# Performance work log

Measured on AMD Instinct MI355X. Metric: run time of the kernel, lower is better.

The kernel has to match this reference:

```python
import jax, jax.numpy as jnp
import numpy as np

E, T, H, I = 8, 1024, 2048, 5632  # experts, tokens/expert, hidden, intermediate


def setup_inputs() -> dict:
    key = jax.random.key(0)
    k1, k2, k3 = jax.random.split(key, 3)
    permuted_hidden_states = jax.random.normal(k1, (E * T, H), dtype=jnp.float32)
    # per-expert weights; linear is x @ W with W[in, out] (same math as nn.Linear with W^T)
    w1 = jax.random.normal(k2, (E, H, 2 * I), dtype=jnp.float32) * 0.02
    w2 = jax.random.normal(k3, (E, I, H), dtype=jnp.float32) * 0.02
    tokens_per_expert = jnp.full((E,), T, dtype=jnp.int32)
    return {
        "permuted_hidden_states": permuted_hidden_states,
        "w1": w1,
        "w2": w2,
        "tokens_per_expert": tokens_per_expert,
    }


def reference(permuted_hidden_states, w1, w2, tokens_per_expert):
    # Tokens are contiguously segmented per expert; with equal counts (static T)
    # the per-expert loop becomes one batched (grouped) GEMM.
    x = permuted_hidden_states.reshape(E, T, H)
    fc1 = jnp.einsum('eth,ehf->etf', x, w1)          # [E, T, 2I]
    a, b = jnp.split(fc1, 2, axis=-1)                # GLU: chunk last dim
    inter = jax.nn.silu(a) * b                       # [E, T, I]
    out = jnp.einsum('eti,eih->eth', inter, w2)      # [E, T, H]
    return out.reshape(E * T, H)
```

## Files before the change

### kernel.cpp

```cpp
#include <hip/hip_runtime.h>
#include <hip/hip_bf16.h>


#define EXPERTS 8
#define TOK     1024
#define HID     2048
#define INTER   5632
#define I2      (2 * INTER)

typedef __bf16 bf16x8 __attribute__((ext_vector_type(8)));
typedef float  f32x4  __attribute__((ext_vector_type(4)));

#define G2(row) ((((row) >> 1) & 3) << 3)

__device__ __forceinline__ unsigned short f2bf(float f) {
    union { float f; unsigned u; } v; v.f = f;
    unsigned r = v.u + 0x7FFFu + ((v.u >> 16) & 1u);
    return (unsigned short)(r >> 16);
}

__device__ __forceinline__ void gload_lds16(const void* g, void* l) {
    __builtin_amdgcn_global_load_lds(
        (const __attribute__((address_space(1))) void*)g,
        (__attribute__((address_space(3))) void*)l, 16, 0, 0);
}

__device__ __forceinline__ bf16x8 ldfrag(const unsigned short* S, int R, int kb) {
    int off = R * 32 + (kb ^ G2(R));
    return *reinterpret_cast<const bf16x8*>(S + off);
}


__global__ __launch_bounds__(256) void k_cvt_x(const float* __restrict__ X,
                                               unsigned short* __restrict__ Xb) {
    size_t base = ((size_t)blockIdx.x * 256 + threadIdx.x) * 8;
    int row = (int)(base >> 11);
    int k   = (int)(base & (HID - 1));
    int kp  = k ^ G2(row);
    float4 v0 = *reinterpret_cast<const float4*>(X + base);
    float4 v1 = *reinterpret_cast<const float4*>(X + base + 4);
    uint4 o;
    o.x = (unsigned)f2bf(v0.x) | ((unsigned)f2bf(v0.y) << 16);
    o.y = (unsigned)f2bf(v0.z) | ((unsigned)f2bf(v0.w) << 16);
    o.z = (unsigned)f2bf(v1.x) | ((unsigned)f2bf(v1.y) << 16);
    o.w = (unsigned)f2bf(v1.z) | ((unsigned)f2bf(v1.w) << 16);
    *reinterpret_cast<uint4*>(Xb + (size_t)row * HID + kp) = o;
}

__global__ __launch_bounds__(256) void k_cvt_w1(const float* __restrict__ W1,
                                                unsigned short* __restrict__ W1T) {
    __shared__ unsigned short lds[64][72];
    const int bid = blockIdx.x;
    const int hb = bid % (HID / 64);
    const int pb = (bid / (HID / 64)) % (I2 / 64);
    const int e  = bid / ((HID / 64) * (I2 / 64));
    const int h0 = hb * 64, p0 = pb * 64, n0 = p0 >> 1;
    const float* w1e = W1 + (size_t)e * HID * I2;
    const int t = threadIdx.x;
#pragma unroll
    for (int it = 0; it < 16; ++it) {
        int lin   = it * 256 + t;
        int n_off = lin & 31;
        int c     = (lin >> 5) & 1;
        int h_off = lin >> 6;
        float v = w1e[(size_t)(h0 + h_off) * I2 + c * INTER + n0 + n_off];
        lds[2 * n_off + c][h_off] = f2bf(v);
    }
    __syncthreads();
    unsigned short* o = W1T + (size_t)e * I2 * HID;
#pragma unroll
    for (int it = 0; it < 4; ++it) {
        int lin = it * 256 + t;
        int r   = lin >> 4;
        int co  = (lin & 15) * 4;
        int cop = co ^ G2(r);
        ushort4 v = *reinterpret_cast<ushort4*>(&lds[r][co]);
        *reinterpret_cast<ushort4*>(o + (size_t)(p0 + r) * HID + h0 + cop) = v;
    }
}

__global__ __launch_bounds__(256) void k_cvt_w2(const float* __restrict__ W2,
                                                unsigned short* __restrict__ W2T) {
    __shared__ unsigned short lds[64][72];
    const int bid = blockIdx.x;
    const int ib = bid % (INTER / 64);
    const int hb = (bid / (INTER / 64)) % (HID / 64);
    const int e  = bid / ((INTER / 64) * (HID / 64));
    const int i0 = ib * 64, h0 = hb * 64;
    const float* w2e = W2 + (size_t)e * INTER * HID;
    const int t = threadIdx.x;
#pragma unroll
    for (int it = 0; it < 16; ++it) {
        int lin   = it * 256 + t;
        int h_off = lin & 63;
        int i_off = lin >> 6;
        float v = w2e[(size_t)(i0 + i_off) * HID + h0 + h_off];
        lds[h_off][i_off] = f2bf(v);
    }
    __syncthreads();
    unsigned short* o = W2T + (size_t)e * HID * INTER;
#pragma unroll
    for (int it = 0; it < 4; ++it) {
        int lin = it * 256 + t;
        int r   = lin >> 4;
        int co  = (lin & 15) * 4;
        int cop = co ^ G2(r);
        ushort4 v = *reinterpret_cast<ushort4*>(&lds[r][co]);
        *reinterpret_cast<ushort4*>(o + (size_t)(h0 + r) * INTER + i0 + cop) = v;
    }
}


__device__ __forceinline__ void stage24(const unsigned short* Ab, const unsigned short* Bb,
                                        int ktot, int k0, unsigned short* buf, int t) {
#pragma unroll
    for (int j = 0; j < 2; ++j) {
        int lin = j * 512 + t;
        int row = lin >> 2;
        int col = (lin & 3) * 8;
        gload_lds16(Ab + (size_t)row * ktot + k0 + col, buf + lin * 8);
    }
    {
        int row = t >> 2;
        int col = (t & 3) * 8;
        gload_lds16(Bb + (size_t)row * ktot + k0 + col, buf + 8192 + t * 8);
    }
}

#define MFMA_BF16(a, b, c) __builtin_amdgcn_mfma_f32_16x16x32_bf16(a, b, c, 0, 0, 0)

__device__ __forceinline__ void gemm_ring3(const unsigned short* Ab, const unsigned short* Bb,
                                           int ktot, int nkt, f32x4 (&acc)[4][4],
                                           unsigned short* lds, int t, int lane,
                                           int wr, int wc) {
    const int cl  = lane & 15;
    const int kb0 = (lane >> 4) << 3;

    stage24(Ab, Bb, ktot, 0,  lds,         t);
    stage24(Ab, Bb, ktot, 32, lds + 12288, t);

    int c_cur = 0, c_n2 = 2;
    for (int kt = 0; kt < nkt; ++kt) {
        if (kt + 1 < nkt) { asm volatile("s_waitcnt vmcnt(3)" ::: "memory"); }
        else              { asm volatile("s_waitcnt vmcnt(0)" ::: "memory"); }
        __builtin_amdgcn_s_barrier();
        asm volatile("" ::: "memory");

        unsigned short* Ac = lds + c_cur * 12288;
        unsigned short* Bc = Ac + 8192;

        if (kt + 2 < nkt)
            stage24(Ab, Bb, ktot, (kt + 2) * 32, lds + c_n2 * 12288, t);

        bf16x8 b[4], a[2];
#pragma unroll
        for (int n = 0; n < 4; ++n)
            b[n] = ldfrag(Bc, wc + n * 16 + cl, kb0);
        a[0] = ldfrag(Ac, wr + cl, kb0);

#pragma unroll
        for (int m = 0; m < 4; ++m) {
            if (m < 3)
                a[(m + 1) & 1] = ldfrag(Ac, wr + (m + 1) * 16 + cl, kb0);
            __builtin_amdgcn_s_setprio(1);
#pragma unroll
            for (int n = 0; n < 4; ++n)
                acc[m][n] = MFMA_BF16(a[m & 1], b[n], acc[m][n]);
            __builtin_amdgcn_s_setprio(0);
        }

        c_cur = (c_cur == 2) ? 0 : c_cur + 1;
        c_n2  = (c_n2  == 2) ? 0 : c_n2  + 1;
    }
}

__global__ __launch_bounds__(512, 4) void k_fc1_r3(const unsigned short* __restrict__ Xb,
                                                   const unsigned short* __restrict__ W1T,
                                                   unsigned short* __restrict__ inter) {
    extern __shared__ unsigned short lds[];
    const int bid = blockIdx.x;
    const int e   = bid & 7;
    const int idx = bid >> 3;
    const int mt  = idx & 3;
    const int nt  = idx >> 2;
    const int t = threadIdx.x, lane = t & 63, w = t >> 6;
    const int wr = (w >> 1) * 64;
    const int wc = (w & 1) * 64;
    const int m0 = e * TOK + mt * 256;
    const int n0 = nt * 128;
    const unsigned short* Ab = Xb  + (size_t)m0 * HID;
    const unsigned short* Bb = W1T + (size_t)e * I2 * HID + (size_t)n0 * HID;

    f32x4 acc[4][4];
#pragma unroll
    for (int i = 0; i < 4; ++i)
#pragma unroll
        for (int j = 0; j < 4; ++j) acc[i][j] = f32x4{0.f, 0.f, 0.f, 0.f};

    gemm_ring3(Ab, Bb, HID, HID / 32, acc, lds, t, lane, wr, wc);

    const int cl = lane & 15;
    const int r0 = (lane >> 4) << 2;
#pragma unroll
    for (int mf = 0; mf < 4; ++mf)
#pragma unroll
        for (int nf = 0; nf < 4; ++nf)
#pragma unroll
            for (int r = 0; r < 4; ++r) {
                float v  = acc[mf][nf][r];
                float pv = __shfl_xor(v, 1);
                if ((lane & 1) == 0) {
                    float s = v / (1.f + __expf(-v)) * pv;
                    int row = m0 + wr + mf * 16 + r0 + r;
                    int pc  = n0 + wc + nf * 16 + cl;
                    int c   = pc >> 1;
                    int c2  = (c & ~31) | ((c & 31) ^ G2(row));
                    inter[(size_t)row * INTER + c2] = f2bf(s);
                }
            }
}

__global__ __launch_bounds__(512, 4) void k_fc2_r3(const unsigned short* __restrict__ A,
                                                   const unsigned short* __restrict__ W2T,
                                                   float* __restrict__ out) {
    extern __shared__ unsigned short lds[];
    const int bid = blockIdx.x;
    const int e   = bid & 7;
    const int idx = bid >> 3;
    const int mt  = idx & 3;
    const int nt  = idx >> 2;
    const int t = threadIdx.x, lane = t & 63, w = t >> 6;
    const int wr = (w >> 1) * 64;
    const int wc = (w & 1) * 64;
    const int m0 = e * TOK + mt * 256;
    const int n0 = nt * 128;
    const unsigned short* Ab = A   + (size_t)m0 * INTER;
    const unsigned short* Bb = W2T + (size_t)e * HID * INTER + (size_t)n0 * INTER;

    f32x4 acc[4][4];
#pragma unroll
    for (int i = 0; i < 4; ++i)
#pragma unroll
        for (int j = 0; j < 4; ++j) acc[i][j] = f32x4{0.f, 0.f, 0.f, 0.f};

    gemm_ring3(Ab, Bb, INTER, INTER / 32, acc, lds, t, lane, wr, wc);

    const int cl = lane & 15;
    const int r0 = (lane >> 4) << 2;
#pragma unroll
    for (int mf = 0; mf < 4; ++mf)
#pragma unroll
        for (int nf = 0; nf < 4; ++nf)
#pragma unroll
            for (int r = 0; r < 4; ++r) {
                int row = m0 + wr + mf * 16 + r0 + r;
                int col = n0 + wc + nf * 16 + cl;
                out[(size_t)row * HID + col] = acc[mf][nf][r];
            }
}


#define BM  128
#define BK  64
#define LDK 72

__global__ __launch_bounds__(256) void k_fc1_glu_fb(
    const float* __restrict__ X, const float* __restrict__ W1,
    unsigned short* __restrict__ inter)
{
    __shared__ unsigned short As[BM][LDK];
    __shared__ unsigned short Bs[128][LDK];
    const int bid = blockIdx.x;
    const int nt  = bid % (INTER / 64);
    const int mt  = (bid / (INTER / 64)) % (TOK / BM);
    const int e   = bid / ((INTER / 64) * (TOK / BM));
    const int t = threadIdx.x, lane = t & 63, w = t >> 6;
    const int m0 = mt * BM;
    const int rowbase = e * TOK + m0;
    f32x4 acc[2][8];
#pragma unroll
    for (int i = 0; i < 2; ++i)
#pragma unroll
        for (int jj = 0; jj < 8; ++jj) acc[i][jj] = f32x4{0.f, 0.f, 0.f, 0.f};
    const int jcol = t & 127;
    const int hf   = t >> 7;
    const int gcol = (jcol < 64) ? (nt * 64 + jcol) : (INTER + nt * 64 + (jcol - 64));
    const float* w1e = W1 + (size_t)e * HID * I2;
    for (int k0 = 0; k0 < HID; k0 += BK) {
#pragma unroll
        for (int it = 0; it < 8; ++it) {
            int lin = it * 256 + t;
            int r   = lin >> 4;
            int kq  = (lin & 15) << 2;
            const float4 v = *reinterpret_cast<const float4*>(
                X + (size_t)(rowbase + r) * HID + k0 + kq);
            ushort4 o;
            o.x = f2bf(v.x); o.y = f2bf(v.y); o.z = f2bf(v.z); o.w = f2bf(v.w);
            *reinterpret_cast<ushort4*>(&As[r][kq]) = o;
        }
#pragma unroll
        for (int it = 0; it < 8; ++it) {
            int kq = hf * 4 + it * 8;
            const float* p = w1e + (size_t)(k0 + kq) * I2 + gcol;
            float v0 = p[0], v1 = p[I2], v2 = p[2 * I2], v3 = p[3 * I2];
            ushort4 o;
            o.x = f2bf(v0); o.y = f2bf(v1); o.z = f2bf(v2); o.w = f2bf(v3);
            *reinterpret_cast<ushort4*>(&Bs[jcol][kq]) = o;
        }
        __syncthreads();
#pragma unroll
        for (int kk = 0; kk < 2; ++kk) {
            const int kb = kk * 32 + ((lane >> 4) << 3);
            bf16x8 a0 = *reinterpret_cast<const bf16x8*>(&As[w * 32 + (lane & 15)][kb]);
            bf16x8 a1 = *reinterpret_cast<const bf16x8*>(&As[w * 32 + 16 + (lane & 15)][kb]);
#pragma unroll
            for (int nf = 0; nf < 8; ++nf) {
                bf16x8 b = *reinterpret_cast<const bf16x8*>(&Bs[nf * 16 + (lane & 15)][kb]);
                acc[0][nf] = MFMA_BF16(a0, b, acc[0][nf]);
                acc[1][nf] = MFMA_BF16(a1, b, acc[1][nf]);
            }
        }
        __syncthreads();
    }
    const int rl0 = w * 32 + ((lane >> 4) << 2);
    const int cl  = lane & 15;
#pragma unroll
    for (int mf = 0; mf < 2; ++mf)
#pragma unroll
        for (int nfa = 0; nfa < 4; ++nfa) {
            f32x4 va = acc[mf][nfa];
            f32x4 vb = acc[mf][nfa + 4];
#pragma unroll
            for (int r = 0; r < 4; ++r) {
                float a = va[r], b = vb[r];
                float s = a / (1.f + __expf(-a)) * b;
                int row = rowbase + rl0 + mf * 16 + r;
                int col = nt * 64 + nfa * 16 + cl;
                inter[(size_t)row * INTER + col] = f2bf(s);
            }
        }
}

__global__ __launch_bounds__(256) void k_fc2_fb(
    const unsigned short* __restrict__ inter, const float* __restrict__ W2,
    float* __restrict__ out)
{
    __shared__ unsigned short As[BM][LDK];
    __shared__ unsigned short Bs[128][LDK];
    const int bid = blockIdx.x;
    const int nt  = bid % (HID / 128);
    const int mt  = (bid / (HID / 128)) % (TOK / BM);
    const int e   = bid / ((HID / 128) * (TOK / BM));
    const int t = threadIdx.x, lane = t & 63, w = t >> 6;
    const int m0 = mt * BM;
    const int rowbase = e * TOK + m0;
    f32x4 acc[2][8];
#pragma unroll
    for (int i = 0; i < 2; ++i)
#pragma unroll
        for (int jj = 0; jj < 8; ++jj) acc[i][jj] = f32x4{0.f, 0.f, 0.f, 0.f};
    const int jcol = t & 127;
    const int hf   = t >> 7;
    const int gcol = nt * 128 + jcol;
    const float* w2e = W2 + (size_t)e * INTER * HID;
    for (int k0 = 0; k0 < INTER; k0 += BK) {
#pragma unroll
        for (int it = 0; it < 4; ++it) {
            int lin = it * 256 + t;
            int r   = lin >> 3;
            int kq  = (lin & 7) << 3;
            uint4 v = *reinterpret_cast<const uint4*>(
                inter + (size_t)(rowbase + r) * INTER + k0 + kq);
            *reinterpret_cast<uint4*>(&As[r][kq]) = v;
        }
#pragma unroll
        for (int it = 0; it < 8; ++it) {
            int kq = hf * 4 + it * 8;
            const float* p = w2e + (size_t)(k0 + kq) * HID + gcol;
            float v0 = p[0], v1 = p[HID], v2 = p[2 * HID], v3 = p[3 * HID];
            ushort4 o;
            o.x = f2bf(v0); o.y = f2bf(v1); o.z = f2bf(v2); o.w = f2bf(v3);
            *reinterpret_cast<ushort4*>(&Bs[jcol][kq]) = o;
        }
        __syncthreads();
#pragma unroll
        for (int kk = 0; kk < 2; ++kk) {
            const int kb = kk * 32 + ((lane >> 4) << 3);
            bf16x8 a0 = *reinterpret_cast<const bf16x8*>(&As[w * 32 + (lane & 15)][kb]);
            bf16x8 a1 = *reinterpret_cast<const bf16x8*>(&As[w * 32 + 16 + (lane & 15)][kb]);
#pragma unroll
            for (int nf = 0; nf < 8; ++nf) {
                bf16x8 b = *reinterpret_cast<const bf16x8*>(&Bs[nf * 16 + (lane & 15)][kb]);
                acc[0][nf] = MFMA_BF16(a0, b, acc[0][nf]);
                acc[1][nf] = MFMA_BF16(a1, b, acc[1][nf]);
            }
        }
        __syncthreads();
    }
    const int rl0 = w * 32 + ((lane >> 4) << 2);
    const int cl  = lane & 15;
#pragma unroll
    for (int mf = 0; mf < 2; ++mf)
#pragma unroll
        for (int nf = 0; nf < 8; ++nf) {
            f32x4 v = acc[mf][nf];
#pragma unroll
            for (int r = 0; r < 4; ++r) {
                int row = rowbase + rl0 + mf * 16 + r;
                int col = nt * 128 + nf * 16 + cl;
                out[(size_t)row * HID + col] = v[r];
            }
        }
}


extern "C" void kernel_launch(void* const* d_in, const int* in_sizes, int n_in,
                              void* d_out, int out_size, void* d_ws, size_t ws_size,
                              hipStream_t stream) {
    const float* X  = (const float*)d_in[0];
    const float* W1 = (const float*)d_in[1];
    const float* W2 = (const float*)d_in[2];
    float* out = (float*)d_out;

    const size_t XB_B  = (size_t)EXPERTS * TOK * HID * 2;
    const size_t W1T_B = (size_t)EXPERTS * I2 * HID * 2;
    const size_t W2T_B = (size_t)EXPERTS * HID * INTER * 2;
    const size_t INT_B = (size_t)EXPERTS * TOK * INTER * 2;
    const size_t need  = XB_B + W1T_B + W2T_B + INT_B;

    if (ws_size >= need) {
        unsigned short* Xb    = (unsigned short*)d_ws;
        unsigned short* w1t   = (unsigned short*)((char*)d_ws + XB_B);
        unsigned short* w2t   = (unsigned short*)((char*)d_ws + XB_B + W1T_B);
        unsigned short* inter = (unsigned short*)((char*)d_ws + XB_B + W1T_B + W2T_B);

        hipFuncSetAttribute((const void*)k_fc1_r3,
            hipFuncAttributeMaxDynamicSharedMemorySize, 73728);
        hipFuncSetAttribute((const void*)k_fc2_r3,
            hipFuncAttributeMaxDynamicSharedMemorySize, 73728);

        dim3 b256(256), b512(512);
        k_cvt_x <<<(EXPERTS * TOK * HID) / (256 * 8), b256, 0, stream>>>(X, Xb);
        k_cvt_w1<<<EXPERTS * (I2 / 64) * (HID / 64),   b256, 0, stream>>>(W1, w1t);
        k_cvt_w2<<<EXPERTS * (HID / 64) * (INTER / 64), b256, 0, stream>>>(W2, w2t);
        k_fc1_r3<<<EXPERTS * 4 * (I2 / 128),  b512, 73728, stream>>>(Xb, w1t, inter);
        k_fc2_r3<<<EXPERTS * 4 * (HID / 128), b512, 73728, stream>>>(inter, w2t, out);
    } else {
        unsigned short* inter = (unsigned short*)d_ws;
        dim3 b256(256);
        k_fc1_glu_fb<<<EXPERTS * (TOK / BM) * (INTER / 64), b256, 0, stream>>>(X, W1, inter);
        k_fc2_fb    <<<EXPERTS * (TOK / BM) * (HID / 128),  b256, 0, stream>>>(inter, W2, out);
    }
}
```

Baseline: 938.6 us.

## Fuse fp32-to-bf16 weight conversion into GEMM B-tile staging, drop transpose kernels

Removes the separate weight transpose/convert kernels and their bf16 workspace copies. Each GEMM now loads the fp32 weight columns straight from global memory into registers, converts them to bf16 and writes them swizzled into LDS, interleaving the GLU columns for fc1. This saves a full read and write pass over the weights. In exchange the GEMM reads twice the bytes per B tile (fp32), and each M-tile block re-converts the same weights. The strided per-thread loads are coalesced across threads along the column.

```diff
diff --git a/kernel.cpp b/kernel.cpp
--- a/kernel.cpp
+++ b/kernel.cpp
@@ -47,135 +47,105 @@
     *reinterpret_cast<uint4*>(Xb + (size_t)row * HID + kp) = o;
 }
 
-__global__ __launch_bounds__(256) void k_cvt_w1(const float* __restrict__ W1,
-                                                unsigned short* __restrict__ W1T) {
-    __shared__ unsigned short lds[64][72];
-    const int bid = blockIdx.x;
-    const int hb = bid % (HID / 64);
-    const int pb = (bid / (HID / 64)) % (I2 / 64);
-    const int e  = bid / ((HID / 64) * (I2 / 64));
-    const int h0 = hb * 64, p0 = pb * 64, n0 = p0 >> 1;
-    const float* w1e = W1 + (size_t)e * HID * I2;
-    const int t = threadIdx.x;
-#pragma unroll
-    for (int it = 0; it < 16; ++it) {
-        int lin   = it * 256 + t;
-        int n_off = lin & 31;
-        int c     = (lin >> 5) & 1;
-        int h_off = lin >> 6;
-        float v = w1e[(size_t)(h0 + h_off) * I2 + c * INTER + n0 + n_off];
-        lds[2 * n_off + c][h_off] = f2bf(v);
-    }
-    __syncthreads();
-    unsigned short* o = W1T + (size_t)e * I2 * HID;
-#pragma unroll
-    for (int it = 0; it < 4; ++it) {
-        int lin = it * 256 + t;
-        int r   = lin >> 4;
-        int co  = (lin & 15) * 4;
-        int cop = co ^ G2(r);
-        ushort4 v = *reinterpret_cast<ushort4*>(&lds[r][co]);
-        *reinterpret_cast<ushort4*>(o + (size_t)(p0 + r) * HID + h0 + cop) = v;
-    }
-}
-
-__global__ __launch_bounds__(256) void k_cvt_w2(const float* __restrict__ W2,
-                                                unsigned short* __restrict__ W2T) {
-    __shared__ unsigned short lds[64][72];
-    const int bid = blockIdx.x;
-    const int ib = bid % (INTER / 64);
-    const int hb = (bid / (INTER / 64)) % (HID / 64);
-    const int e  = bid / ((INTER / 64) * (HID / 64));
-    const int i0 = ib * 64, h0 = hb * 64;
-    const float* w2e = W2 + (size_t)e * INTER * HID;
-    const int t = threadIdx.x;
-#pragma unroll
-    for (int it = 0; it < 16; ++it) {
-        int lin   = it * 256 + t;
-        int h_off = lin & 63;
-        int i_off = lin >> 6;
-        float v = w2e[(size_t)(i0 + i_off) * HID + h0 + h_off];
-        lds[h_off][i_off] = f2bf(v);
-    }
-    __syncthreads();
-    unsigned short* o = W2T + (size_t)e * HID * INTER;
-#pragma unroll
-    for (int it = 0; it < 4; ++it) {
-        int lin = it * 256 + t;
-        int r   = lin >> 4;
-        int co  = (lin & 15) * 4;
-        int cop = co ^ G2(r);
-        ushort4 v = *reinterpret_cast<ushort4*>(&lds[r][co]);
-        *reinterpret_cast<ushort4*>(o + (size_t)(h0 + r) * INTER + i0 + cop) = v;
-    }
-}
-
-
-__device__ __forceinline__ void stage24(const unsigned short* Ab, const unsigned short* Bb,
-                                        int ktot, int k0, unsigned short* buf, int t) {
+
+template <int KTOT>
+__device__ __forceinline__ void stageA(const unsigned short* Ab, int k0,
+                                       unsigned short* buf, int t) {
 #pragma unroll
     for (int j = 0; j < 2; ++j) {
         int lin = j * 512 + t;
         int row = lin >> 2;
         int col = (lin & 3) * 8;
-        gload_lds16(Ab + (size_t)row * ktot + k0 + col, buf + lin * 8);
-    }
-    {
-        int row = t >> 2;
-        int col = (t & 3) * 8;
-        gload_lds16(Bb + (size_t)row * ktot + k0 + col, buf + 8192 + t * 8);
-    }
+        gload_lds16(Ab + (size_t)row * KTOT + k0 + col, buf + lin * 8);
+    }
+}
+
+template <int LDW>
+__device__ __forceinline__ void loadB(const float* W, int gcol, int k0, int kq8,
+                                      float (&r)[8]) {
+    const float* p = W + (size_t)(k0 + kq8) * LDW + gcol;
+#pragma unroll
+    for (int j = 0; j < 8; ++j) r[j] = p[(size_t)j * LDW];
+}
+
+__device__ __forceinline__ void writeB(unsigned short* Bl, int pcl, int kq8,
+                                       float (&r)[8]) {
+    uint4 o;
+    o.x = (unsigned)f2bf(r[0]) | ((unsigned)f2bf(r[1]) << 16);
+    o.y = (unsigned)f2bf(r[2]) | ((unsigned)f2bf(r[3]) << 16);
+    o.z = (unsigned)f2bf(r[4]) | ((unsigned)f2bf(r[5]) << 16);
+    o.w = (unsigned)f2bf(r[6]) | ((unsigned)f2bf(r[7]) << 16);
+    *reinterpret_cast<uint4*>(Bl + pcl * 32 + (kq8 ^ G2(pcl))) = o;
 }
 
 #define MFMA_BF16(a, b, c) __builtin_amdgcn_mfma_f32_16x16x32_bf16(a, b, c, 0, 0, 0)
 
-__device__ __forceinline__ void gemm_ring3(const unsigned short* Ab, const unsigned short* Bb,
-                                           int ktot, int nkt, f32x4 (&acc)[4][4],
+__device__ __forceinline__ void compute_tile(const unsigned short* Ac,
+                                             const unsigned short* Bc,
+                                             f32x4 (&acc)[4][4],
+                                             int wr, int wc, int cl, int kb0) {
+    bf16x8 b[4], a[2];
+#pragma unroll
+    for (int n = 0; n < 4; ++n)
+        b[n] = ldfrag(Bc, wc + n * 16 + cl, kb0);
+    a[0] = ldfrag(Ac, wr + cl, kb0);
+#pragma unroll
+    for (int m = 0; m < 4; ++m) {
+        if (m < 3)
+            a[(m + 1) & 1] = ldfrag(Ac, wr + (m + 1) * 16 + cl, kb0);
+        __builtin_amdgcn_s_setprio(1);
+#pragma unroll
+        for (int n = 0; n < 4; ++n)
+            acc[m][n] = MFMA_BF16(a[m & 1], b[n], acc[m][n]);
+        __builtin_amdgcn_s_setprio(0);
+    }
+}
+
+template <int KTOT, int LDW>
+__device__ __forceinline__ void gemm_ring3(const unsigned short* Ab, const float* W,
+                                           int gcol, f32x4 (&acc)[4][4],
                                            unsigned short* lds, int t, int lane,
                                            int wr, int wc) {
     const int cl  = lane & 15;
     const int kb0 = (lane >> 4) << 3;
-
-    stage24(Ab, Bb, ktot, 0,  lds,         t);
-    stage24(Ab, Bb, ktot, 32, lds + 12288, t);
-
-    int c_cur = 0, c_n2 = 2;
+    const int pcl = t & 127;
+    const int kq8 = (t >> 7) * 8;
+    const int nkt = KTOT / 32;
+
+    unsigned short* p0 = lds;
+    unsigned short* p1 = lds + 12288;
+    unsigned short* p2 = lds + 24576;
+
+    float r[8];
+    stageA<KTOT>(Ab, 0, p0, t);
+    loadB<LDW>(W, gcol, 0, kq8, r);
+    stageA<KTOT>(Ab, 32, p1, t);
+    asm volatile("s_waitcnt vmcnt(2)" ::: "memory");
+    writeB(p0 + 8192, pcl, kq8, r);
+    asm volatile("s_waitcnt lgkmcnt(0)" ::: "memory");
+    __builtin_amdgcn_s_barrier();
+    asm volatile("" ::: "memory");
+
     for (int kt = 0; kt < nkt; ++kt) {
-        if (kt + 1 < nkt) { asm volatile("s_waitcnt vmcnt(3)" ::: "memory"); }
-        else              { asm volatile("s_waitcnt vmcnt(0)" ::: "memory"); }
-        __builtin_amdgcn_s_barrier();
-        asm volatile("" ::: "memory");
-
-        unsigned short* Ac = lds + c_cur * 12288;
-        unsigned short* Bc = Ac + 8192;
-
-        if (kt + 2 < nkt)
-            stage24(Ab, Bb, ktot, (kt + 2) * 32, lds + c_n2 * 12288, t);
-
-        bf16x8 b[4], a[2];
-#pragma unroll
-        for (int n = 0; n < 4; ++n)
-            b[n] = ldfrag(Bc, wc + n * 16 + cl, kb0);
-        a[0] = ldfrag(Ac, wr + cl, kb0);
-
-#pragma unroll
-        for (int m = 0; m < 4; ++m) {
-            if (m < 3)
-                a[(m + 1) & 1] = ldfrag(Ac, wr + (m + 1) * 16 + cl, kb0);
-            __builtin_amdgcn_s_setprio(1);
-#pragma unroll
-            for (int n = 0; n < 4; ++n)
-                acc[m][n] = MFMA_BF16(a[m & 1], b[n], acc[m][n]);
-            __builtin_amdgcn_s_setprio(0);
-        }
-
-        c_cur = (c_cur == 2) ? 0 : c_cur + 1;
-        c_n2  = (c_n2  == 2) ? 0 : c_n2  + 1;
-    }
-}
-
-__global__ __launch_bounds__(512, 4) void k_fc1_r3(const unsigned short* __restrict__ Xb,
-                                                   const unsigned short* __restrict__ W1T,
+        if (kt + 1 < nkt) loadB<LDW>(W, gcol, (kt + 1) * 32, kq8, r);
+        if (kt + 2 < nkt) stageA<KTOT>(Ab, (kt + 2) * 32, p2, t);
+
+        compute_tile(p0, p0 + 8192, acc, wr, wc, cl, kb0);
+
+        if (kt + 1 < nkt) {
+            if (kt + 2 < nkt) { asm volatile("s_waitcnt vmcnt(2)" ::: "memory"); }
+            else              { asm volatile("s_waitcnt vmcnt(0)" ::: "memory"); }
+            writeB(p1 + 8192, pcl, kq8, r);
+            asm volatile("s_waitcnt lgkmcnt(0)" ::: "memory");
+            __builtin_amdgcn_s_barrier();
+            asm volatile("" ::: "memory");
+        }
+        unsigned short* tmp = p0; p0 = p1; p1 = p2; p2 = tmp;
+    }
+}
+
+__global__ __launch_bounds__(512, 4) void k_fc1_r4(const unsigned short* __restrict__ Xb,
+                                                   const float* __restrict__ W1,
                                                    unsigned short* __restrict__ inter) {
     extern __shared__ unsigned short lds[];
     const int bid = blockIdx.x;
@@ -188,8 +158,10 @@
     const int wc = (w & 1) * 64;
     const int m0 = e * TOK + mt * 256;
     const int n0 = nt * 128;
-    const unsigned short* Ab = Xb  + (size_t)m0 * HID;
-    const unsigned short* Bb = W1T + (size_t)e * I2 * HID + (size_t)n0 * HID;
+    const unsigned short* Ab = Xb + (size_t)m0 * HID;
+    const float* W = W1 + (size_t)e * HID * I2;
+    const int pc   = n0 + (t & 127);
+    const int gcol = (pc & 1) * INTER + (pc >> 1);
 
     f32x4 acc[4][4];
 #pragma unroll
@@ -197,7 +169,7 @@
 #pragma unroll
         for (int j = 0; j < 4; ++j) acc[i][j] = f32x4{0.f, 0.f, 0.f, 0.f};
 
-    gemm_ring3(Ab, Bb, HID, HID / 32, acc, lds, t, lane, wr, wc);
+    gemm_ring3<HID, I2>(Ab, W, gcol, acc, lds, t, lane, wr, wc);
 
     const int cl = lane & 15;
     const int r0 = (lane >> 4) << 2;
@@ -212,16 +184,16 @@
                 if ((lane & 1) == 0) {
                     float s = v / (1.f + __expf(-v)) * pv;
                     int row = m0 + wr + mf * 16 + r0 + r;
-                    int pc  = n0 + wc + nf * 16 + cl;
-                    int c   = pc >> 1;
+                    int pcc = n0 + wc + nf * 16 + cl;
+                    int c   = pcc >> 1;
                     int c2  = (c & ~31) | ((c & 31) ^ G2(row));
                     inter[(size_t)row * INTER + c2] = f2bf(s);
                 }
             }
 }
 
-__global__ __launch_bounds__(512, 4) void k_fc2_r3(const unsigned short* __restrict__ A,
-                                                   const unsigned short* __restrict__ W2T,
+__global__ __launch_bounds__(512, 4) void k_fc2_r4(const unsigned short* __restrict__ A,
+                                                   const float* __restrict__ W2,
                                                    float* __restrict__ out) {
     extern __shared__ unsigned short lds[];
     const int bid = blockIdx.x;
@@ -234,8 +206,9 @@
     const int wc = (w & 1) * 64;
     const int m0 = e * TOK + mt * 256;
     const int n0 = nt * 128;
-    const unsigned short* Ab = A   + (size_t)m0 * INTER;
-    const unsigned short* Bb = W2T + (size_t)e * HID * INTER + (size_t)n0 * INTER;
+    const unsigned short* Ab = A + (size_t)m0 * INTER;
+    const float* W = W2 + (size_t)e * INTER * HID;
+    const int gcol = n0 + (t & 127);
 
     f32x4 acc[4][4];
 #pragma unroll
@@ -243,7 +216,7 @@
 #pragma unroll
         for (int j = 0; j < 4; ++j) acc[i][j] = f32x4{0.f, 0.f, 0.f, 0.f};
 
-    gemm_ring3(Ab, Bb, INTER, INTER / 32, acc, lds, t, lane, wr, wc);
+    gemm_ring3<INTER, HID>(Ab, W, gcol, acc, lds, t, lane, wr, wc);
 
     const int cl = lane & 15;
     const int r0 = (lane >> 4) << 2;
@@ -423,28 +396,22 @@
     float* out = (float*)d_out;
 
     const size_t XB_B  = (size_t)EXPERTS * TOK * HID * 2;
-    const size_t W1T_B = (size_t)EXPERTS * I2 * HID * 2;
-    const size_t W2T_B = (size_t)EXPERTS * HID * INTER * 2;
     const size_t INT_B = (size_t)EXPERTS * TOK * INTER * 2;
-    const size_t need  = XB_B + W1T_B + W2T_B + INT_B;
+    const size_t need  = XB_B + INT_B;
 
     if (ws_size >= need) {
         unsigned short* Xb    = (unsigned short*)d_ws;
-        unsigned short* w1t   = (unsigned short*)((char*)d_ws + XB_B);
-        unsigned short* w2t   = (unsigned short*)((char*)d_ws + XB_B + W1T_B);
-        unsigned short* inter = (unsigned short*)((char*)d_ws + XB_B + W1T_B + W2T_B);
-
-        hipFuncSetAttribute((const void*)k_fc1_r3,
+        unsigned short* inter = (unsigned short*)((char*)d_ws + XB_B);
+
+        hipFuncSetAttribute((const void*)k_fc1_r4,
             hipFuncAttributeMaxDynamicSharedMemorySize, 73728);
-        hipFuncSetAttribute((const void*)k_fc2_r3,
+        hipFuncSetAttribute((const void*)k_fc2_r4,
             hipFuncAttributeMaxDynamicSharedMemorySize, 73728);
 
         dim3 b256(256), b512(512);
         k_cvt_x <<<(EXPERTS * TOK * HID) / (256 * 8), b256, 0, stream>>>(X, Xb);
-        k_cvt_w1<<<EXPERTS * (I2 / 64) * (HID / 64),   b256, 0, stream>>>(W1, w1t);
-        k_cvt_w2<<<EXPERTS * (HID / 64) * (INTER / 64), b256, 0, stream>>>(W2, w2t);
-        k_fc1_r3<<<EXPERTS * 4 * (I2 / 128),  b512, 73728, stream>>>(Xb, w1t, inter);
-        k_fc2_r3<<<EXPERTS * 4 * (HID / 128), b512, 73728, stream>>>(inter, w2t, out);
+        k_fc1_r4<<<EXPERTS * 4 * (I2 / 128),  b512, 73728, stream>>>(Xb, W1, inter);
+        k_fc2_r4<<<EXPERTS * 4 * (HID / 128), b512, 73728, stream>>>(inter, W2, out);
     } else {
         unsigned short* inter = (unsigned short*)d_ws;
         dim3 b256(256);
```

After: 981.6 us. 4.6% more time.
